# Kernel tuning notes

Hardware: AMD Instinct MI355X
Metric: run time of the kernel (lower is better)

Reference implementation:

```python
import jax, jax.numpy as jnp
import numpy as np

N, FIN, FOUT = 4096, 512, 256
ALPHA = 0.2          # LeakyReLU negative slope
NEG_INF = -9e15      # mask value from the torch source


def setup_inputs() -> dict:
    key = jax.random.key(0)
    ks = jax.random.split(key, 11)
    h = jax.random.normal(ks[0], (N, FIN), dtype=jnp.float32)
    adj_n = jax.random.randint(ks[1], (N, N), 0, 2, dtype=jnp.int32)
    adj_d = jax.random.randint(ks[2], (N, N), 0, 2, dtype=jnp.int32)
    G_nd = jax.random.normal(ks[3], (2, N, FOUT), dtype=jnp.float32)
    # learned parameters (xavier-ish scale)
    W_n = jax.random.normal(ks[4], (FIN, FOUT), dtype=jnp.float32) * 0.05
    a1_n = jax.random.normal(ks[5], (FOUT, 1), dtype=jnp.float32) * 0.05
    a2_n = jax.random.normal(ks[6], (FOUT, 1), dtype=jnp.float32) * 0.05
    W_d = jax.random.normal(ks[7], (FIN, FOUT), dtype=jnp.float32) * 0.05
    a1_d = jax.random.normal(ks[8], (FOUT, 1), dtype=jnp.float32) * 0.05
    a2_d = jax.random.normal(ks[9], (FOUT, 1), dtype=jnp.float32) * 0.05
    scale = jnp.zeros((1,), dtype=jnp.float32)
    return {"h": h, "adj_n": adj_n, "adj_d": adj_d, "G_nd": G_nd,
            "W_n": W_n, "a1_n": a1_n, "a2_n": a2_n,
            "W_d": W_d, "a1_d": a1_d, "a2_d": a2_d, "scale": scale}


def _gat(h, adj, W, a1, a2):
    # Wh: [N, FOUT]
    Wh = h @ W
    # outer-sum attention logits: e[i,j] = leakyrelu(Wh_i.a1 + Wh_j.a2)
    e = jax.nn.leaky_relu((Wh @ a1) + (Wh @ a2).T, negative_slope=ALPHA)  # [N, N]
    att = jnp.where(adj > 0, e, jnp.float32(NEG_INF))
    att = jax.nn.softmax(att, axis=-1)
    # dropout is identity in eval mode
    return jax.nn.elu(att @ Wh)  # [N, FOUT]


def reference(h, adj_n, adj_d, G_nd, W_n, a1_n, a2_n, W_d, a1_d, a2_d, scale):
    f_n_S = _gat(h, adj_n, W_n, a1_n, a2_n)
    f_d_S = _gat(h, adj_d, W_d, a1_d, a2_d)
    # The G_nd cross-attention branch (f_nd_C) in the torch source is computed
    # but never used in the returned value; omitted here (jit would DCE it).
    return f_n_S + f_d_S
```

## Files before the change

kernel.cpp:

```cpp
#include <hip/hip_runtime.h>
#include <hip/hip_bf16.h>

#define N_NODES 4096
#define FIN     512
#define FOUT    256
#define NSPLIT  4
#define NTILES  ((N_NODES / NSPLIT) / 64)
#define ITILE   128

typedef __attribute__((ext_vector_type(8))) short bf16x8s;
typedef __attribute__((ext_vector_type(4))) float f32x4;
typedef __attribute__((ext_vector_type(8))) unsigned short u16x8;
typedef unsigned short u16;
typedef unsigned int   u32;

__device__ inline u16 f2b(float f) {
    union { float f; unsigned int u; } v; v.f = f;
    unsigned int r = v.u + 0x7fffu + ((v.u >> 16) & 1u);
    return (u16)(r >> 16);
}

__device__ inline u16 f2b_fast(float f) {
    return __bfloat16_as_ushort(__float2bfloat16(f));
}

__global__ __launch_bounds__(256) void prep_kernel(
    const float* __restrict__ h, const float* __restrict__ Wn,
    const float* __restrict__ Wd,
    u16* __restrict__ hb, u16* __restrict__ WTb, float* __restrict__ s12)
{
    __shared__ u16 tl[64 * 72];
    const int t = threadIdx.x;
    const int bid = blockIdx.x;

    if (bid < 1024) {
        int idx = (bid * 256 + t) * 8;
        float4 f0 = *(const float4*)&h[idx];
        float4 f1 = *(const float4*)&h[idx + 4];
        u16x8 o;
        o[0]=f2b(f0.x); o[1]=f2b(f0.y); o[2]=f2b(f0.z); o[3]=f2b(f0.w);
        o[4]=f2b(f1.x); o[5]=f2b(f1.y); o[6]=f2b(f1.z); o[7]=f2b(f1.w);
        *(u16x8*)&hb[idx] = o;
    } else if (bid < 1088) {
        int id = bid - 1024;
        int kx = id & 7, ny = (id >> 3) & 3, b = id >> 5;
        const float* W = b ? Wd : Wn;
        int k0 = kx * 64, n0 = ny * 64;
        int kr = t >> 2, nc0 = (t & 3) * 16;
        const float* src = W + (size_t)(k0 + kr) * FOUT + n0 + nc0;
        #pragma unroll
        for (int jv = 0; jv < 4; ++jv) {
            float4 f = *(const float4*)(src + jv * 4);
            tl[(nc0 + jv * 4 + 0) * 72 + kr] = f2b(f.x);
            tl[(nc0 + jv * 4 + 1) * 72 + kr] = f2b(f.y);
            tl[(nc0 + jv * 4 + 2) * 72 + kr] = f2b(f.z);
            tl[(nc0 + jv * 4 + 3) * 72 + kr] = f2b(f.w);
        }
        __syncthreads();
        int n = t >> 2, kc0 = (t & 3) * 16;
        u16* dst = WTb + ((size_t)b << 17) + (size_t)(n0 + n) * FIN + k0 + kc0;
        *(uint4*)dst       = *(uint4*)&tl[n * 72 + kc0];
        *(uint4*)(dst + 8) = *(uint4*)&tl[n * 72 + kc0 + 8];
    } else {
        float4 z = {0.f, 0.f, 0.f, 0.f};
        float4* p4 = (float4*)s12;
        #pragma unroll
        for (int k = 0; k < 16; ++k) p4[k * 256 + t] = z;
    }
}

__global__ __launch_bounds__(256) void wh_gemm_kernel(
    const u16* __restrict__ hb, const u16* __restrict__ WTb,
    const float* __restrict__ a1n, const float* __restrict__ a2n,
    const float* __restrict__ a1d, const float* __restrict__ a2d,
    u16* __restrict__ WhT, float* __restrict__ s1, float* __restrict__ s2)
{
    __shared__ u16 a_lds[64 * 256];
    __shared__ u16 b_lds[64 * 256];

    const int t = threadIdx.x, lane = t & 63, w = t >> 6;
    const int q = lane >> 4, ln = lane & 15;
    const int i0 = blockIdx.x * 64, n0 = blockIdx.y * 64, b = blockIdx.z;
    const u16* wt = WTb + ((size_t)b << 17);

    f32x4 acc[4];
    #pragma unroll
    for (int i = 0; i < 4; ++i) acc[i] = (f32x4){0.f, 0.f, 0.f, 0.f};

    for (int kt = 0; kt < 2; ++kt) {
        const int k0 = kt * 256;
        __syncthreads();
        #pragma unroll
        for (int it = 0; it < 8; ++it) {
            int chunk = it * 256 + t;
            int r = chunk >> 5, kc = chunk & 31;
            const u16* g = hb + (size_t)(i0 + r) * FIN + k0 + ((kc ^ (r & 31)) * 8);
            u16* l = a_lds + (it * 256 + w * 64) * 8;
            __builtin_amdgcn_global_load_lds(
                (const __attribute__((address_space(1))) void*)g,
                (__attribute__((address_space(3))) void*)l, 16, 0, 0);
        }
        #pragma unroll
        for (int it = 0; it < 8; ++it) {
            int chunk = it * 256 + t;
            int n = chunk >> 5, kc = chunk & 31;
            const u16* g = wt + (size_t)(n0 + n) * FIN + k0 + ((kc ^ (n & 31)) * 8);
            u16* l = b_lds + (it * 256 + w * 64) * 8;
            __builtin_amdgcn_global_load_lds(
                (const __attribute__((address_space(1))) void*)g,
                (__attribute__((address_space(3))) void*)l, 16, 0, 0);
        }
        __syncthreads();
        #pragma unroll
        for (int ks = 0; ks < 8; ++ks) {
            const int c = ks * 4 + q;
            const int ar = w * 16 + ln;
            bf16x8s af = *(const bf16x8s*)&a_lds[ar * 256 + ((c ^ (ar & 31)) * 8)];
            #pragma unroll
            for (int nt = 0; nt < 4; ++nt) {
                const int nr = nt * 16 + ln;
                bf16x8s bfv = *(const bf16x8s*)&b_lds[nr * 256 + ((c ^ (nr & 31)) * 8)];
                acc[nt] = __builtin_amdgcn_mfma_f32_16x16x32_bf16(af, bfv, acc[nt], 0, 0, 0);
            }
        }
    }

    {
        const float* a1 = b ? a1d : a1n;
        const float* a2 = b ? a2d : a2n;
        float s1p[4] = {0.f, 0.f, 0.f, 0.f};
        float s2p[4] = {0.f, 0.f, 0.f, 0.f};
        #pragma unroll
        for (int nt = 0; nt < 4; ++nt) {
            float va1 = a1[n0 + nt * 16 + ln];
            float va2 = a2[n0 + nt * 16 + ln];
            #pragma unroll
            for (int r = 0; r < 4; ++r) {
                s1p[r] += acc[nt][r] * va1;
                s2p[r] += acc[nt][r] * va2;
            }
        }
        #pragma unroll
        for (int r = 0; r < 4; ++r) {
            #pragma unroll
            for (int off = 8; off >= 1; off >>= 1) {
                s1p[r] += __shfl_xor(s1p[r], off);
                s2p[r] += __shfl_xor(s2p[r], off);
            }
            if (ln == 0) {
                int row = i0 + w * 16 + q * 4 + r;
                atomicAdd(&s1[b * N_NODES + row], s1p[r]);
                atomicAdd(&s2[b * N_NODES + row], s2p[r]);
            }
        }
    }

    __syncthreads();
    #pragma unroll
    for (int nt = 0; nt < 4; ++nt)
        #pragma unroll
        for (int r = 0; r < 4; ++r)
            a_lds[(nt * 16 + ln) * 72 + (w * 16 + q * 4 + r)] = f2b(acc[nt][r]);
    __syncthreads();
    {
        const int nl = t >> 2, is = (t & 3) * 16;
        u16* dst = WhT + ((size_t)b << 20) + (size_t)(n0 + nl) * N_NODES + i0 + is;
        *(uint4*)dst       = *(uint4*)&a_lds[nl * 72 + is];
        *(uint4*)(dst + 8) = *(uint4*)&a_lds[nl * 72 + is + 8];
    }
}

__global__ __launch_bounds__(1024) void attn_kernel(
    const int* __restrict__ adj_n, const int* __restrict__ adj_d,
    const u16* __restrict__ WhT,
    const float* __restrict__ s1, const float* __restrict__ s2,
    float* __restrict__ num_ws, float* __restrict__ den_ws)
{
    __shared__ u16 wht_lds[256 * 64];
    __shared__ u16 p_lds[128 * 64];

    const int t = threadIdx.x, lane = t & 63, w = t >> 6;
    const int q = lane >> 4, ln = lane & 15;
    const int ih = w >> 2;
    const int nq = w & 3;
    const int b = blockIdx.z, split = blockIdx.y;
    const int i0 = blockIdx.x * ITILE;

    const int* adjb = b ? adj_d : adj_n;
    const u16* whtB = WhT + ((size_t)b << 20);
    const float* s1b = s1 + b * N_NODES;
    const float* s2b = s2 + b * N_NODES;

    const int pr = t >> 3;
    const int cw = t & 7;
    const int pc = cw * 8;
    const float s1v = s1b[i0 + pr];
    const size_t arow = (size_t)(i0 + pr) * N_NODES + pc;
    const int swp = (cw ^ (pr & 7)) * 8;

    float den0 = 0.f;

    f32x4 acc[2][4];
    #pragma unroll
    for (int mt = 0; mt < 2; ++mt)
        #pragma unroll
        for (int nt = 0; nt < 4; ++nt) acc[mt][nt] = (f32x4){0.f, 0.f, 0.f, 0.f};

    const int jbase = split * (N_NODES / NSPLIT);

    int4 a0_pf = *(const int4*)&adjb[arow + jbase];
    int4 a1_pf = *(const int4*)&adjb[arow + jbase + 4];
    float4 sv0_pf = *(const float4*)&s2b[jbase + pc];
    float4 sv1_pf = *(const float4*)&s2b[jbase + pc + 4];

    for (int jt = 0; jt < NTILES; ++jt) {
        const int j0 = jbase + jt * 64;
        __syncthreads();
        #pragma unroll
        for (int it = 0; it < 2; ++it) {
            int chunk = it * 1024 + t;
            int n = chunk >> 3, kc = chunk & 7;
            const u16* g = whtB + (size_t)n * N_NODES + j0 + ((kc ^ (n & 7)) * 8);
            u16* l = wht_lds + (it * 1024 + w * 64) * 8;
            __builtin_amdgcn_global_load_lds(
                (const __attribute__((address_space(1))) void*)g,
                (__attribute__((address_space(3))) void*)l, 16, 0, 0);
        }
        int4 a0 = a0_pf, a1 = a1_pf;
        float4 sv0 = sv0_pf, sv1 = sv1_pf;
        if (jt < NTILES - 1) {
            const int jn = j0 + 64;
            a0_pf = *(const int4*)&adjb[arow + jn];
            a1_pf = *(const int4*)&adjb[arow + jn + 4];
            sv0_pf = *(const float4*)&s2b[jn + pc];
            sv1_pf = *(const float4*)&s2b[jn + pc + 4];
        }
        int v[8] = {a0.x, a0.y, a0.z, a0.w, a1.x, a1.y, a1.z, a1.w};
        float svf[8] = {sv0.x, sv0.y, sv0.z, sv0.w, sv1.x, sv1.y, sv1.z, sv1.w};
        float d = 0.f;
        u16x8 pk;
        #pragma unroll
        for (int jj = 0; jj < 8; ++jj) {
            float x = s1v + svf[jj];
            float p = (v[jj] > 0) ? __expf(fmaxf(x, 0.2f * x)) : 0.f;
            d += p;
            pk[jj] = f2b_fast(p);
        }
        d += __shfl_down(d, 4, 8);
        d += __shfl_down(d, 2, 8);
        d += __shfl_down(d, 1, 8);
        if ((t & 7) == 0) den0 += d;
        *(u16x8*)&p_lds[pr * 64 + swp] = pk;
        __syncthreads();
        #pragma unroll
        for (int ks = 0; ks < 2; ++ks) {
            int sw = ((ks * 4 + q) ^ (ln & 7)) * 8;
            bf16x8s af0 = *(const bf16x8s*)&p_lds[(ih * 32 + 0 * 16 + ln) * 64 + sw];
            bf16x8s af1 = *(const bf16x8s*)&p_lds[(ih * 32 + 1 * 16 + ln) * 64 + sw];
            #pragma unroll
            for (int nt = 0; nt < 4; ++nt) {
                bf16x8s bfv = *(const bf16x8s*)&wht_lds[(nq * 64 + nt * 16 + ln) * 64 + sw];
                acc[0][nt] = __builtin_amdgcn_mfma_f32_16x16x32_bf16(af0, bfv, acc[0][nt], 0, 0, 0);
                acc[1][nt] = __builtin_amdgcn_mfma_f32_16x16x32_bf16(af1, bfv, acc[1][nt], 0, 0, 0);
            }
        }
    }
    const size_t pbase = (size_t)(b * NSPLIT + split) * N_NODES;
    #pragma unroll
    for (int mt = 0; mt < 2; ++mt)
        #pragma unroll
        for (int r = 0; r < 4; ++r) {
            int row = ih * 32 + mt * 16 + q * 4 + r;
            #pragma unroll
            for (int nt = 0; nt < 4; ++nt)
                num_ws[(pbase + i0 + row) * FOUT + nq * 64 + nt * 16 + ln] = acc[mt][nt][r];
        }
    if ((t & 7) == 0) den_ws[pbase + i0 + pr] = den0;
}

__global__ __launch_bounds__(256) void reduce_kernel(
    const float* __restrict__ num_ws, const float* __restrict__ den_ws,
    float* __restrict__ out)
{
    int gid = blockIdx.x * 256 + threadIdx.x;
    int i = gid >> 6;
    int f4 = (gid & 63) * 4;
    float4 o = {0.f, 0.f, 0.f, 0.f};
    #pragma unroll
    for (int b = 0; b < 2; ++b) {
        float4 num = {0.f, 0.f, 0.f, 0.f};
        float den = 0.f;
        #pragma unroll
        for (int s = 0; s < NSPLIT; ++s) {
            const float4 v = *(const float4*)&num_ws[((size_t)(b * NSPLIT + s) * N_NODES + i) * FOUT + f4];
            num.x += v.x; num.y += v.y; num.z += v.z; num.w += v.w;
            den += den_ws[(size_t)(b * NSPLIT + s) * N_NODES + i];
        }
        float inv = 1.0f / den;
        float e0 = num.x * inv, e1 = num.y * inv, e2 = num.z * inv, e3 = num.w * inv;
        o.x += (e0 > 0.f) ? e0 : expm1f(e0);
        o.y += (e1 > 0.f) ? e1 : expm1f(e1);
        o.z += (e2 > 0.f) ? e2 : expm1f(e2);
        o.w += (e3 > 0.f) ? e3 : expm1f(e3);
    }
    *(float4*)&out[(size_t)i * FOUT + f4] = o;
}

extern "C" void kernel_launch(void* const* d_in, const int* in_sizes, int n_in,
                              void* d_out, int out_size, void* d_ws, size_t ws_size,
                              hipStream_t stream) {
    const float* h    = (const float*)d_in[0];
    const int*   adjn = (const int*)d_in[1];
    const int*   adjd = (const int*)d_in[2];
    const float* Wn   = (const float*)d_in[4];
    const float* a1n  = (const float*)d_in[5];
    const float* a2n  = (const float*)d_in[6];
    const float* Wd   = (const float*)d_in[7];
    const float* a1d  = (const float*)d_in[8];
    const float* a2d  = (const float*)d_in[9];

    char* ws = (char*)d_ws;
    u16*  WhT  = (u16*)ws;
    float* s1  = (float*)(ws + ((size_t)8 << 20));
    float* s2  = s1 + 2 * N_NODES;
    float* den = s2 + 2 * N_NODES;
    u16*  hb   = (u16*)(ws + ((size_t)8 << 20) + ((size_t)256 << 10));
    u16*  WTb  = (u16*)(ws + ((size_t)12 << 20) + ((size_t)256 << 10));
    float* num = (float*)(ws + ((size_t)8 << 20) + ((size_t)256 << 10));

    prep_kernel<<<1089, 256, 0, stream>>>(h, Wn, Wd, hb, WTb, s1);
    wh_gemm_kernel<<<dim3(64, 4, 2), 256, 0, stream>>>(hb, WTb, a1n, a2n, a1d, a2d, WhT, s1, s2);
    attn_kernel<<<dim3(N_NODES / ITILE, NSPLIT, 2), 1024, 0, stream>>>(adjn, adjd, WhT, s1, s2, num, den);
    reduce_kernel<<<1024, 256, 0, stream>>>(num, den, (float*)d_out);
}
```

Baseline: 214.5 us.

## Accumulate attention partials with atomics and double the key split count

The attention kernel now atomically adds its partial numerator and denominator into one zero-initialised buffer per branch, instead of writing a separate slice per split. The split count rises from 4 to 8, launching twice as many blocks with half the key range each. The prep kernel gets extra blocks to zero the larger accumulator region, and the reduce kernel reads a single slice. This removes the reduce kernel's multi-slice reads, in exchange for float atomic traffic and contention, nondeterministic summation order, and the accumulator re-zeroing done on every call.

```diff
diff --git a/kernel.cpp b/kernel.cpp
--- a/kernel.cpp
+++ b/kernel.cpp
@@ -4,7 +4,7 @@
 #define N_NODES 4096
 #define FIN     512
 #define FOUT    256
-#define NSPLIT  4
+#define NSPLIT  8
 #define NTILES  ((N_NODES / NSPLIT) / 64)
 #define ITILE   128
 
@@ -62,10 +62,15 @@
         *(uint4*)dst       = *(uint4*)&tl[n * 72 + kc0];
         *(uint4*)(dst + 8) = *(uint4*)&tl[n * 72 + kc0 + 8];
     } else {
+        const int zid = bid - 1088;
         float4 z = {0.f, 0.f, 0.f, 0.f};
         float4* p4 = (float4*)s12;
-        #pragma unroll
-        for (int k = 0; k < 16; ++k) p4[k * 256 + t] = z;
+        const int base = zid * 4096;
+        #pragma unroll
+        for (int k = 0; k < 16; ++k) {
+            int idx = base + k * 256 + t;
+            if (idx < 530432) p4[idx] = z;
+        }
     }
 }
 
@@ -174,7 +179,7 @@
     const int* __restrict__ adj_n, const int* __restrict__ adj_d,
     const u16* __restrict__ WhT,
     const float* __restrict__ s1, const float* __restrict__ s2,
-    float* __restrict__ num_ws, float* __restrict__ den_ws)
+    float* __restrict__ num, float* __restrict__ den)
 {
     __shared__ u16 wht_lds[256 * 64];
     __shared__ u16 p_lds[128 * 64];
@@ -265,7 +270,7 @@
             }
         }
     }
-    const size_t pbase = (size_t)(b * NSPLIT + split) * N_NODES;
+    float* numB = num + (size_t)b * N_NODES * FOUT;
     #pragma unroll
     for (int mt = 0; mt < 2; ++mt)
         #pragma unroll
@@ -273,13 +278,14 @@
             int row = ih * 32 + mt * 16 + q * 4 + r;
             #pragma unroll
             for (int nt = 0; nt < 4; ++nt)
-                num_ws[(pbase + i0 + row) * FOUT + nq * 64 + nt * 16 + ln] = acc[mt][nt][r];
-        }
-    if ((t & 7) == 0) den_ws[pbase + i0 + pr] = den0;
+                atomicAdd(&numB[(size_t)(i0 + row) * FOUT + nq * 64 + nt * 16 + ln],
+                          acc[mt][nt][r]);
+        }
+    if ((t & 7) == 0) atomicAdd(&den[b * N_NODES + i0 + pr], den0);
 }
 
 __global__ __launch_bounds__(256) void reduce_kernel(
-    const float* __restrict__ num_ws, const float* __restrict__ den_ws,
+    const float* __restrict__ num, const float* __restrict__ den,
     float* __restrict__ out)
 {
     int gid = blockIdx.x * 256 + threadIdx.x;
@@ -288,16 +294,9 @@
     float4 o = {0.f, 0.f, 0.f, 0.f};
     #pragma unroll
     for (int b = 0; b < 2; ++b) {
-        float4 num = {0.f, 0.f, 0.f, 0.f};
-        float den = 0.f;
-        #pragma unroll
-        for (int s = 0; s < NSPLIT; ++s) {
-            const float4 v = *(const float4*)&num_ws[((size_t)(b * NSPLIT + s) * N_NODES + i) * FOUT + f4];
-            num.x += v.x; num.y += v.y; num.z += v.z; num.w += v.w;
-            den += den_ws[(size_t)(b * NSPLIT + s) * N_NODES + i];
-        }
-        float inv = 1.0f / den;
-        float e0 = num.x * inv, e1 = num.y * inv, e2 = num.z * inv, e3 = num.w * inv;
+        const float4 v = *(const float4*)&num[((size_t)b * N_NODES + i) * FOUT + f4];
+        float inv = 1.0f / den[b * N_NODES + i];
+        float e0 = v.x * inv, e1 = v.y * inv, e2 = v.z * inv, e3 = v.w * inv;
         o.x += (e0 > 0.f) ? e0 : expm1f(e0);
         o.y += (e1 > 0.f) ? e1 : expm1f(e1);
         o.z += (e2 > 0.f) ? e2 : expm1f(e2);
@@ -324,11 +323,11 @@
     float* s1  = (float*)(ws + ((size_t)8 << 20));
     float* s2  = s1 + 2 * N_NODES;
     float* den = s2 + 2 * N_NODES;
-    u16*  hb   = (u16*)(ws + ((size_t)8 << 20) + ((size_t)256 << 10));
-    u16*  WTb  = (u16*)(ws + ((size_t)12 << 20) + ((size_t)256 << 10));
-    float* num = (float*)(ws + ((size_t)8 << 20) + ((size_t)256 << 10));
-
-    prep_kernel<<<1089, 256, 0, stream>>>(h, Wn, Wd, hb, WTb, s1);
+    float* num = den + 2 * N_NODES;
+    u16*  hb   = (u16*)(ws + ((size_t)20 << 20));
+    u16*  WTb  = (u16*)(ws + ((size_t)24 << 20));
+
+    prep_kernel<<<1218, 256, 0, stream>>>(h, Wn, Wd, hb, WTb, s1);
     wh_gemm_kernel<<<dim3(64, 4, 2), 256, 0, stream>>>(hb, WTb, a1n, a2n, a1d, a2d, WhT, s1, s2);
     attn_kernel<<<dim3(N_NODES / ITILE, NSPLIT, 2), 1024, 0, stream>>>(adjn, adjd, WhT, s1, s2, num, den);
     reduce_kernel<<<1024, 256, 0, stream>>>(num, den, (float*)d_out);
```

Result: slower. 240.3 us (+12.0%).
